# Performance work log

Hardware: AMD Instinct MI355X
Metric: run time of the kernel (lower is better)

## Reference

```python
import jax, jax.numpy as jnp
import numpy as np

DIN = 1024
DOUT = 1024


def setup_inputs() -> dict:
    key = jax.random.key(0)
    kx, kq, kk, kv = jax.random.split(key, 4)
    B, T = 4, 2048
    x = jax.random.normal(kx, (B, T, DIN), dtype=jnp.float32)
    # nn.Linear weights are (dout, din); init like PyTorch default scale
    s = 1.0 / np.sqrt(DIN)
    Wq = jax.random.uniform(kq, (DOUT, DIN), minval=-s, maxval=s, dtype=jnp.float32)
    Wk = jax.random.uniform(kk, (DOUT, DIN), minval=-s, maxval=s, dtype=jnp.float32)
    Wv = jax.random.uniform(kv, (DOUT, DIN), minval=-s, maxval=s, dtype=jnp.float32)
    return {"x": x, "Wq": Wq, "Wk": Wk, "Wv": Wv}


def reference(x, Wq, Wk, Wv):
    B, T, _ = x.shape
    q = jnp.einsum('btd,ed->bte', x, Wq)
    k = jnp.einsum('btd,ed->bte', x, Wk)
    v = jnp.einsum('btd,ed->bte', x, Wv)
    attn = jnp.einsum('bqe,bke->bqk', q, k)  # [B, T, T]
    # Faithful to source: masked_fill result is discarded, so the causal mask
    # is a MULTIPLICATIVE tril of ones (upper triangle logits become 0, not -inf).
    mask = jnp.tril(jnp.ones((T, T), dtype=attn.dtype))
    attn = attn * mask
    # Faithful to source: scale by sqrt(last dim of attn) = sqrt(T), not sqrt(d).
    attn = jax.nn.softmax(attn / jnp.sqrt(jnp.asarray(T, attn.dtype)), axis=-1)
    return jnp.einsum('bqk,bke->bqe', attn, v)
```

## Files before the change

kernel.cpp:

```cpp
#include <hip/hip_runtime.h>
#include <stdint.h>

#define BB 4
#define TT 2048
#define DD 1024
#define NX (BB*TT*DD)
#define NW (DD*DD)
#define SCALE 0.022097086912079608f
#define SCALEI 2.157918643757774e-5f
#define UNSCALE 7.689469810104304e-6f
#define Q8F 2.4606299212598425e-4f

typedef short v8s __attribute__((ext_vector_type(8)));
typedef float v4f __attribute__((ext_vector_type(4)));
typedef int   v4i __attribute__((ext_vector_type(4)));
typedef uint8_t u8;

typedef const void __attribute__((address_space(1))) *as1_cvp;
typedef void __attribute__((address_space(3))) *as3_vp;

__device__ __forceinline__ short f2bf(float f) {
    union { float f; uint32_t u; } x; x.f = f;
    uint32_t r = x.u + 0x7fffu + ((x.u >> 16) & 1u);
    return (short)(r >> 16);
}
__device__ __forceinline__ float bf2f(short s) {
    union { uint32_t u; float f; } x; x.u = ((uint32_t)(uint16_t)s) << 16;
    return x.f;
}

__device__ __forceinline__ void gl_lds16(const void* g, const void* lds_wave_base) {
    __builtin_amdgcn_global_load_lds(
        (as1_cvp)(uintptr_t)g,
        (as3_vp)(uint32_t)(uintptr_t)lds_wave_base,
        16, 0, 0);
}

__device__ __forceinline__ v8s frag_read(const short* lds, int row, int cg) {
    return *(const v8s*)(lds + row * 64 + ((cg ^ (row & 7)) << 3));
}

#define WAITV(N) asm volatile("s_waitcnt vmcnt(" #N ")" ::: "memory")

__device__ __forceinline__ void stage128_512(const short* __restrict__ g, int lda,
                                             short* lds, int tid) {
    #pragma unroll
    for (int s = 0; s < 2; s++) {
        int t = s * 512 + tid;
        int r = t >> 3, c = t & 7, cg = c ^ (r & 7);
        gl_lds16(g + (size_t)r * lda + cg * 8, lds + s * 4096 + (tid >> 6) * 512);
    }
}

__device__ __forceinline__ void stA8(const u8* __restrict__ g, u8* lds, int tid) {
    #pragma unroll
    for (int s = 0; s < 2; s++) {
        int t = s * 512 + tid;
        int r = t >> 3, c = t & 7, cg = c ^ (r & 7);
        gl_lds16(g + (size_t)r * 1024 + cg * 16, lds + s * 8192 + (tid >> 6) * 1024);
    }
}
__device__ __forceinline__ void stB8(const u8* __restrict__ g, u8* lds, int tid, int p) {
    #pragma unroll
    for (int s = 0; s < 2; s++) {
        int t = s * 512 + tid;
        int r = t >> 3, c = t & 7, cg = c ^ (r & 7);
        int grow = ((r >> 5) << 6) + p * 32 + (r & 31);
        gl_lds16(g + (size_t)grow * 1024 + cg * 16, lds + s * 8192 + (tid >> 6) * 1024);
    }
}
__device__ __forceinline__ v4i frag16(const u8* lds, int row, int c) {
    return *(const v4i*)(lds + row * 128 + ((c ^ (row & 7)) << 4));
}

__device__ __forceinline__ void stage64(const u8* __restrict__ g, u8* lds, int tid) {
    int r = tid >> 2, c = tid & 3;
    gl_lds16(g + (size_t)r * 1024 + c * 16, lds + (tid >> 6) * 1024);
}
__device__ __forceinline__ v4i fragK64(const u8* lds, int row, int gq) {
    return *(const v4i*)(lds + row * 64 + gq * 16);
}

__global__ void k_convert(const float* __restrict__ x, const float* __restrict__ Wq,
                          const float* __restrict__ Wk, const float* __restrict__ Wv,
                          u8* __restrict__ dst8, float* __restrict__ rowsum) {
    int i = blockIdx.x * 256 + threadIdx.x;
    if (i < BB * TT) rowsum[i] = (float)((15 - ((i & 2047) >> 7)) * 128);
    size_t base = (size_t)i * 4;
    const float* src; size_t off; float sc; bool clip;
    if (base < NX)               { src = x;  off = base; sc = 32.f; clip = true; }
    else if (base < NX + NW)     { src = Wq; off = base - NX; sc = 4064.f; clip = false; }
    else if (base < NX + 2*(size_t)NW) { src = Wk; off = base - NX - NW; sc = 4064.f; clip = false; }
    else                         { src = Wv; off = base - NX - 2*(size_t)NW; sc = 4064.f; clip = false; }
    float4 f = *(const float4*)(src + off);
    float a0 = f.x * sc, a1 = f.y * sc, a2 = f.z * sc, a3 = f.w * sc;
    if (clip) {
        a0 = fminf(fmaxf(a0, -127.f), 127.f);
        a1 = fminf(fmaxf(a1, -127.f), 127.f);
        a2 = fminf(fmaxf(a2, -127.f), 127.f);
        a3 = fminf(fmaxf(a3, -127.f), 127.f);
    }
    int q0 = __float2int_rn(a0), q1 = __float2int_rn(a1);
    int q2 = __float2int_rn(a2), q3 = __float2int_rn(a3);
    uint32_t w = (uint32_t)(q0 & 255) | ((uint32_t)(q1 & 255) << 8) |
                 ((uint32_t)(q2 & 255) << 16) | ((uint32_t)(q3 & 255) << 24);
    *(uint32_t*)(dst8 + base) = w;
}

__global__ __launch_bounds__(512, 2) void k_qkv(const u8* __restrict__ xb,
                                                const u8* __restrict__ wb,
                                                u8* __restrict__ q8,
                                                u8* __restrict__ k8,
                                                short* __restrict__ vt) {
    int h = blockIdx.x;
    int w = (h & 7) * 96 + (h >> 3);
    int which = w >> 8, rem = w & 255, ntile = rem >> 6, mtile = rem & 63;
    int m0 = mtile * 128, n0 = ntile * 256;
    const u8* Ag = xb + (size_t)m0 * 1024;
    const u8* Bg = wb + (size_t)which * NW + (size_t)n0 * 1024;
    __shared__ __align__(16) u8 SH[98304];
    int tid = threadIdx.x, lane = tid & 63, wave = tid >> 6;
    int wm = wave >> 2, wn = wave & 3;
    int lr = lane & 15, lq = lane >> 4;
    int arow = wm * 64 + lr;
    int brow = wn * 32 + lr;
    v4i acc[4][4];
    #pragma unroll
    for (int i = 0; i < 4; i++)
        #pragma unroll
        for (int j = 0; j < 4; j++) acc[i][j] = (v4i){0, 0, 0, 0};

    stA8(Ag, SH,         tid);
    stB8(Bg, SH + 16384, tid, 0);
    stB8(Bg, SH + 32768, tid, 1);

    #pragma unroll
    for (int t = 0; t < 8; ++t) {
        u8* S  = SH + (t & 1) * 49152;
        u8* Sn = SH + ((t + 1) & 1) * 49152;
        const u8* Agn = Ag + (t + 1) * 128;
        const u8* Bgn = Bg + (t + 1) * 128;
        WAITV(2);
        __builtin_amdgcn_s_barrier();
        v4i af[4][2], bf[2][2];
        #pragma unroll
        for (int i = 0; i < 4; i++)
            #pragma unroll
            for (int kh = 0; kh < 2; kh++) af[i][kh] = frag16(S, arow + i * 16, kh * 4 + lq);
        #pragma unroll
        for (int jj = 0; jj < 2; jj++)
            #pragma unroll
            for (int kh = 0; kh < 2; kh++) bf[jj][kh] = frag16(S + 16384, brow + jj * 16, kh * 4 + lq);
        if (t < 7) {
            stA8(Agn, Sn,         tid);
            stB8(Bgn, Sn + 16384, tid, 0);
        }
        __builtin_amdgcn_s_setprio(1);
        #pragma unroll
        for (int kh = 0; kh < 2; kh++)
            #pragma unroll
            for (int i = 0; i < 4; i++)
                #pragma unroll
                for (int jj = 0; jj < 2; jj++)
                    acc[i][jj] = __builtin_amdgcn_mfma_i32_16x16x64_i8(af[i][kh], bf[jj][kh], acc[i][jj], 0, 0, 0);
        __builtin_amdgcn_s_setprio(0);
        if (t < 7) { WAITV(4); }
        else       { WAITV(0); }
        __builtin_amdgcn_s_barrier();
        v4i bg2[2][2];
        #pragma unroll
        for (int jj = 0; jj < 2; jj++)
            #pragma unroll
            for (int kh = 0; kh < 2; kh++) bg2[jj][kh] = frag16(S + 32768, brow + jj * 16, kh * 4 + lq);
        if (t < 7) stB8(Bgn, Sn + 32768, tid, 1);
        __builtin_amdgcn_s_setprio(1);
        #pragma unroll
        for (int kh = 0; kh < 2; kh++)
            #pragma unroll
            for (int i = 0; i < 4; i++)
                #pragma unroll
                for (int jj = 0; jj < 2; jj++)
                    acc[i][2 + jj] = __builtin_amdgcn_mfma_i32_16x16x64_i8(af[i][kh], bg2[jj][kh], acc[i][2 + jj], 0, 0, 0);
        __builtin_amdgcn_s_setprio(0);
    }

    if (which == 2) {
        #pragma unroll
        for (int a = 0; a < 4; a++)
            #pragma unroll
            for (int b = 0; b < 4; b++)
                #pragma unroll
                for (int r = 0; r < 4; r++) {
                    int row = m0 + wm * 64 + a * 16 + lq * 4 + r;
                    int col = n0 + wn * 64 + b * 16 + lr;
                    int bb = row >> 11, tt2 = row & 2047;
                    vt[((size_t)bb << 21) + ((size_t)col << 11) + tt2] =
                        f2bf((float)acc[a][b][r] * UNSCALE);
                }
    } else {
        u8* outp = (which == 0) ? q8 : k8;
        #pragma unroll
        for (int a = 0; a < 4; a++)
            #pragma unroll
            for (int b = 0; b < 4; b++)
                #pragma unroll
                for (int r = 0; r < 4; r++) {
                    int row = m0 + wm * 64 + a * 16 + lq * 4 + r;
                    int col = n0 + wn * 64 + b * 16 + lr;
                    float v = (float)acc[a][b][r] * Q8F;
                    v = fminf(fmaxf(v, -127.f), 127.f);
                    outp[(size_t)row * 1024 + col] = (u8)(__float2int_rn(v) & 255);
                }
    }
}

__global__ void k_ts1(const short* __restrict__ vt, float* __restrict__ TSpart) {
    int g = blockIdx.x * 256 + threadIdx.x;
    int b = g >> 14, jt = (g >> 10) & 15, e = g & 1023;
    const short* row = vt + ((size_t)b << 21) + ((size_t)e << 11) + jt * 128;
    float s = 0.f;
    #pragma unroll
    for (int c = 0; c < 16; c++) {
        uint4 u = *(const uint4*)(row + c * 8);
        const short* hp = (const short*)&u;
        #pragma unroll
        for (int z = 0; z < 8; z++) s += bf2f(hp[z]);
    }
    TSpart[g] = s;
}
__global__ void k_ts2(const float* __restrict__ TSpart, float* __restrict__ TS) {
    int g = blockIdx.x * 256 + threadIdx.x;
    int b = g >> 10, e = g & 1023;
    float acc = 0.f;
    TS[(size_t)(b * 17 + 16) * 1024 + e] = 0.f;
    for (int jt = 15; jt >= 0; jt--) {
        acc += TSpart[(size_t)(b * 16 + jt) * 1024 + e];
        TS[(size_t)(b * 17 + jt) * 1024 + e] = acc;
    }
}

__global__ __launch_bounds__(512, 4) void k_pk(const u8* __restrict__ q8,
                                               const u8* __restrict__ k8,
                                               short* __restrict__ P,
                                               float* __restrict__ rowsum) {
    int pidx = blockIdx.x, b = blockIdx.z;
    int qt = 0;
    while ((qt + 1) * (qt + 2) / 2 <= pidx) qt++;
    int kt = pidx - qt * (qt + 1) / 2;
    int r0 = qt * 128;
    const u8* Ag = q8 + ((size_t)b * 2048 + r0) * 1024;
    const u8* Bg = k8 + ((size_t)b * 2048 + (size_t)kt * 128) * 1024;
    __shared__ __align__(16) u8 SH[49152];
    int tid = threadIdx.x, lane = tid & 63, wave = tid >> 6;
    int wm2 = wave >> 2, wn4 = wave & 3;
    int lr = lane & 15, lq = lane >> 4;
    v4i acc[4][2];
    #pragma unroll
    for (int i = 0; i < 4; i++)
        #pragma unroll
        for (int j = 0; j < 2; j++) acc[i][j] = (v4i){0, 0, 0, 0};

    stage64(Ag,      SH,                tid);
    stage64(Bg,      SH + 8192,         tid);
    stage64(Ag + 64, SH + 16384,        tid);
    stage64(Bg + 64, SH + 16384 + 8192, tid);

    #pragma unroll
    for (int it = 0; it < 16; ++it) {
        if (it + 1 < 16) { WAITV(2); }
        else             { WAITV(0); }
        __builtin_amdgcn_s_barrier();
        if (it + 2 < 16) {
            u8* Sn = SH + ((it + 2) % 3) * 16384;
            stage64(Ag + (it + 2) * 64, Sn,        tid);
            stage64(Bg + (it + 2) * 64, Sn + 8192, tid);
        }
        const u8* S = SH + (it % 3) * 16384;
        v4i af[4], bf[2];
        #pragma unroll
        for (int i = 0; i < 4; i++) af[i] = fragK64(S, wm2 * 64 + i * 16 + lr, lq);
        #pragma unroll
        for (int j = 0; j < 2; j++) bf[j] = fragK64(S + 8192, wn4 * 32 + j * 16 + lr, lq);
        __builtin_amdgcn_s_setprio(1);
        #pragma unroll
        for (int i = 0; i < 4; i++)
            #pragma unroll
            for (int j = 0; j < 2; j++)
                acc[i][j] = __builtin_amdgcn_mfma_i32_16x16x64_i8(af[i], bf[j], acc[i][j], 0, 0, 0);
        __builtin_amdgcn_s_setprio(0);
    }
    short* Pb = P + ((size_t)b << 22);
    float rs[4][4];
    #pragma unroll
    for (int i = 0; i < 4; i++)
        #pragma unroll
        for (int r = 0; r < 4; r++) rs[i][r] = 0.f;
    #pragma unroll
    for (int i = 0; i < 4; i++)
        #pragma unroll
        for (int j = 0; j < 2; j++)
            #pragma unroll
            for (int r = 0; r < 4; r++) {
                int qi = r0 + wm2 * 64 + i * 16 + lq * 4 + r;
                int kj = kt * 128 + wn4 * 32 + j * 16 + lr;
                float p = (kj <= qi) ? __expf((float)acc[i][j][r] * SCALEI) : 1.0f;
                Pb[(size_t)qi * 2048 + kj] = f2bf(p);
                rs[i][r] += p;
            }
    #pragma unroll
    for (int m = 1; m < 16; m <<= 1)
        #pragma unroll
        for (int i = 0; i < 4; i++)
            #pragma unroll
            for (int r = 0; r < 4; r++) rs[i][r] += __shfl_xor(rs[i][r], m);
    if (lr == 0)
        #pragma unroll
        for (int i = 0; i < 4; i++)
            #pragma unroll
            for (int r = 0; r < 4; r++)
                atomicAdd(&rowsum[b * 2048 + r0 + wm2 * 64 + i * 16 + lq * 4 + r], rs[i][r]);
}

__global__ __launch_bounds__(512, 2) void k_pv(const short* __restrict__ P,
                                               const short* __restrict__ vt,
                                               const float* __restrict__ rowsum,
                                               const float* __restrict__ TS,
                                               float* __restrict__ out) {
    int et = blockIdx.x, p = blockIdx.y, b = blockIdx.z;
    const short* Bg = vt + ((size_t)b << 21) + (size_t)et * 128 * 2048;
    __shared__ __align__(16) short SH[49152];
    int tid = threadIdx.x, lane = tid & 63, wave = tid >> 6;
    int wm2 = wave >> 2, wn4 = wave & 3;
    int lr = lane & 15, lq = lane >> 4;

    #pragma unroll
    for (int ph = 0; ph < 2; ph++) {
        int qt = ph ? p : 15 - p;
        int r0 = qt * 128;
        int iters = 2 * (qt + 1);
        const short* Ag = P + ((size_t)b << 22) + (size_t)r0 * 2048;
        v4f acc[4][2];
        #pragma unroll
        for (int i = 0; i < 4; i++)
            #pragma unroll
            for (int j = 0; j < 2; j++) acc[i][j] = (v4f){0.f, 0.f, 0.f, 0.f};

        stage128_512(Ag,      2048, SH,                tid);
        stage128_512(Bg,      2048, SH + 8192,         tid);
        stage128_512(Ag + 64, 2048, SH + 16384,        tid);
        stage128_512(Bg + 64, 2048, SH + 16384 + 8192, tid);

        for (int it = 0; it < iters; ++it) {
            if (it + 1 < iters) { WAITV(4); }
            else                { WAITV(0); }
            __builtin_amdgcn_s_barrier();
            if (it + 2 < iters) {
                short* Sn = SH + ((it + 2) % 3) * 16384;
                stage128_512(Ag + (it + 2) * 64, 2048, Sn,        tid);
                stage128_512(Bg + (it + 2) * 64, 2048, Sn + 8192, tid);
            }
            short* S = SH + (it % 3) * 16384;
            v8s af[4][2], bf[2][2];
            #pragma unroll
            for (int i = 0; i < 4; i++)
                #pragma unroll
                for (int kk = 0; kk < 2; kk++) af[i][kk] = frag_read(S, wm2 * 64 + i * 16 + lr, kk * 4 + lq);
            #pragma unroll
            for (int j = 0; j < 2; j++)
                #pragma unroll
                for (int kk = 0; kk < 2; kk++) bf[j][kk] = frag_read(S + 8192, wn4 * 32 + j * 16 + lr, kk * 4 + lq);
            __builtin_amdgcn_s_setprio(1);
            #pragma unroll
            for (int kk = 0; kk < 2; kk++)
                #pragma unroll
                for (int i = 0; i < 4; i++)
                    #pragma unroll
                    for (int j = 0; j < 2; j++)
                        acc[i][j] = __builtin_amdgcn_mfma_f32_16x16x32_bf16(af[i][kk], bf[j][kk], acc[i][j], 0, 0, 0);
            __builtin_amdgcn_s_setprio(0);
        }
        const float* tsrow = TS + (size_t)(b * 17 + qt + 1) * 1024;
        #pragma unroll
        for (int i = 0; i < 4; i++)
            #pragma unroll
            for (int j = 0; j < 2; j++)
                #pragma unroll
                for (int r = 0; r < 4; r++) {
                    int row = r0 + wm2 * 64 + i * 16 + lq * 4 + r;
                    int col = et * 128 + wn4 * 32 + j * 16 + lr;
                    float o = (acc[i][j][r] + tsrow[col]) / rowsum[b * 2048 + row];
                    out[((size_t)(b * 2048 + row) << 10) + col] = o;
                }
        __builtin_amdgcn_s_barrier();
    }
}

extern "C" void kernel_launch(void* const* d_in, const int* in_sizes, int n_in,
                              void* d_out, int out_size, void* d_ws, size_t ws_size,
                              hipStream_t stream) {
    const float* x  = (const float*)d_in[0];
    const float* Wq = (const float*)d_in[1];
    const float* Wk = (const float*)d_in[2];
    const float* Wv = (const float*)d_in[3];
    float* out = (float*)d_out;
    char* ws = (char*)d_ws;

    u8*    xb8    = (u8*)(ws + 0);
    u8*    q8     = (u8*)(ws + 11534336);
    u8*    k8     = (u8*)(ws + 19922944);
    short* vt     = (short*)(ws + 28311552);
    short* P      = (short*)(ws + 45088768);
    float* rowsum = (float*)(ws + 78643200);
    float* TSpart = (float*)(ws + 78675968);
    float* TS     = (float*)(ws + 78938112);

    k_convert<<<11264, 256, 0, stream>>>(x, Wq, Wk, Wv, xb8, rowsum);
    k_qkv<<<dim3(768, 1, 1), 512, 0, stream>>>(xb8, xb8 + NX, q8, k8, vt);
    k_ts1<<<256, 256, 0, stream>>>(vt, TSpart);
    k_ts2<<<16, 256, 0, stream>>>(TSpart, TS);
    k_pk<<<dim3(136, 1, 4), 512, 0, stream>>>(q8, k8, P, rowsum);
    k_pv<<<dim3(8, 8, 4), 512, 0, stream>>>(P, vt, rowsum, TS, out);
}
```

Measured before the change: 202.3 us.

## Quantize P and V to int8 and run PV matmul with int8 MFMA

The P matrix written by k_pk is stored as biased int8 (p*64 - 128) instead of bf16. V gets an extra int8 copy scaled by 48, with bias-correction column sums (TQ) computed alongside TS. k_pv then uses i8 MFMA with K=128 per iteration and reconstructs the numerator from the int accumulator, the TQ bias term and TS. This halves the bytes of the P write/read and the PV staging, and uses the faster int8 matrix path. The cost is much coarser quantization of attention weights and values, plus extra stores in the QKV epilogue and k_ts1.

```diff
diff --git a/kernel.cpp b/kernel.cpp
--- a/kernel.cpp
+++ b/kernel.cpp
@@ -10,6 +10,9 @@
 #define SCALEI 2.157918643757774e-5f
 #define UNSCALE 7.689469810104304e-6f
 #define Q8F 2.4606299212598425e-4f
+#define VQ 48.0f
+#define PVF (1.0f/3072.0f)
+#define TQF (1.0f/24.0f)
 
 typedef short v8s __attribute__((ext_vector_type(8)));
 typedef float v4f __attribute__((ext_vector_type(4)));
@@ -27,6 +30,14 @@
 __device__ __forceinline__ float bf2f(short s) {
     union { uint32_t u; float f; } x; x.u = ((uint32_t)(uint16_t)s) << 16;
     return x.f;
+}
+__device__ __forceinline__ int bsum(uint32_t w) {
+#if __has_builtin(__builtin_amdgcn_sdot4)
+    return __builtin_amdgcn_sdot4((int)w, 0x01010101, 0, false);
+#else
+    return (int)(signed char)(w & 255) + (int)(signed char)((w >> 8) & 255) +
+           (int)(signed char)((w >> 16) & 255) + (int)(signed char)((w >> 24) & 255);
+#endif
 }
 
 __device__ __forceinline__ void gl_lds16(const void* g, const void* lds_wave_base) {
@@ -36,28 +47,15 @@
         16, 0, 0);
 }
 
-__device__ __forceinline__ v8s frag_read(const short* lds, int row, int cg) {
-    return *(const v8s*)(lds + row * 64 + ((cg ^ (row & 7)) << 3));
-}
-
 #define WAITV(N) asm volatile("s_waitcnt vmcnt(" #N ")" ::: "memory")
 
-__device__ __forceinline__ void stage128_512(const short* __restrict__ g, int lda,
-                                             short* lds, int tid) {
+__device__ __forceinline__ void stage128B(const u8* __restrict__ g, int lda,
+                                          u8* lds, int tid) {
     #pragma unroll
     for (int s = 0; s < 2; s++) {
         int t = s * 512 + tid;
         int r = t >> 3, c = t & 7, cg = c ^ (r & 7);
-        gl_lds16(g + (size_t)r * lda + cg * 8, lds + s * 4096 + (tid >> 6) * 512);
-    }
-}
-
-__device__ __forceinline__ void stA8(const u8* __restrict__ g, u8* lds, int tid) {
-    #pragma unroll
-    for (int s = 0; s < 2; s++) {
-        int t = s * 512 + tid;
-        int r = t >> 3, c = t & 7, cg = c ^ (r & 7);
-        gl_lds16(g + (size_t)r * 1024 + cg * 16, lds + s * 8192 + (tid >> 6) * 1024);
+        gl_lds16(g + (size_t)r * lda + cg * 16, lds + s * 8192 + (tid >> 6) * 1024);
     }
 }
 __device__ __forceinline__ void stB8(const u8* __restrict__ g, u8* lds, int tid, int p) {
@@ -111,7 +109,8 @@
                                                 const u8* __restrict__ wb,
                                                 u8* __restrict__ q8,
                                                 u8* __restrict__ k8,
-                                                short* __restrict__ vt) {
+                                                short* __restrict__ vt,
+                                                u8* __restrict__ vt8) {
     int h = blockIdx.x;
     int w = (h & 7) * 96 + (h >> 3);
     int which = w >> 8, rem = w & 255, ntile = rem >> 6, mtile = rem & 63;
@@ -130,7 +129,7 @@
         #pragma unroll
         for (int j = 0; j < 4; j++) acc[i][j] = (v4i){0, 0, 0, 0};
 
-    stA8(Ag, SH,         tid);
+    stage128B(Ag, 1024, SH, tid);
     stB8(Bg, SH + 16384, tid, 0);
     stB8(Bg, SH + 32768, tid, 1);
 
@@ -152,7 +151,7 @@
             #pragma unroll
             for (int kh = 0; kh < 2; kh++) bf[jj][kh] = frag16(S + 16384, brow + jj * 16, kh * 4 + lq);
         if (t < 7) {
-            stA8(Agn, Sn,         tid);
+            stage128B(Agn, 1024, Sn,  tid);
             stB8(Bgn, Sn + 16384, tid, 0);
         }
         __builtin_amdgcn_s_setprio(1);
@@ -188,15 +187,25 @@
         #pragma unroll
         for (int a = 0; a < 4; a++)
             #pragma unroll
-            for (int b = 0; b < 4; b++)
-                #pragma unroll
-                for (int r = 0; r < 4; r++) {
-                    int row = m0 + wm * 64 + a * 16 + lq * 4 + r;
-                    int col = n0 + wn * 64 + b * 16 + lr;
-                    int bb = row >> 11, tt2 = row & 2047;
-                    vt[((size_t)bb << 21) + ((size_t)col << 11) + tt2] =
-                        f2bf((float)acc[a][b][r] * UNSCALE);
-                }
+            for (int b = 0; b < 4; b++) {
+                int row0 = m0 + wm * 64 + a * 16 + lq * 4;
+                int col  = n0 + wn * 64 + b * 16 + lr;
+                int bb = row0 >> 11, tt0 = row0 & 2047;
+                size_t idx = ((size_t)bb << 21) + ((size_t)col << 11) + tt0;
+                float v0 = (float)acc[a][b][0] * UNSCALE;
+                float v1 = (float)acc[a][b][1] * UNSCALE;
+                float v2 = (float)acc[a][b][2] * UNSCALE;
+                float v3 = (float)acc[a][b][3] * UNSCALE;
+                short4 hv; hv.x = f2bf(v0); hv.y = f2bf(v1); hv.z = f2bf(v2); hv.w = f2bf(v3);
+                *(short4*)(vt + idx) = hv;
+                int c0 = __float2int_rn(fminf(fmaxf(v0 * VQ, -127.f), 127.f));
+                int c1 = __float2int_rn(fminf(fmaxf(v1 * VQ, -127.f), 127.f));
+                int c2 = __float2int_rn(fminf(fmaxf(v2 * VQ, -127.f), 127.f));
+                int c3 = __float2int_rn(fminf(fmaxf(v3 * VQ, -127.f), 127.f));
+                uint32_t pw = (uint32_t)(c0 & 255) | ((uint32_t)(c1 & 255) << 8) |
+                              ((uint32_t)(c2 & 255) << 16) | ((uint32_t)(c3 & 255) << 24);
+                *(uint32_t*)(vt8 + idx) = pw;
+            }
     } else {
         u8* outp = (which == 0) ? q8 : k8;
         #pragma unroll
@@ -214,7 +223,8 @@
     }
 }
 
-__global__ void k_ts1(const short* __restrict__ vt, float* __restrict__ TSpart) {
+__global__ void k_ts1(const short* __restrict__ vt, const u8* __restrict__ vt8,
+                      float* __restrict__ TSpart, float* __restrict__ TQpart) {
     int g = blockIdx.x * 256 + threadIdx.x;
     int b = g >> 14, jt = (g >> 10) & 15, e = g & 1023;
     const short* row = vt + ((size_t)b << 21) + ((size_t)e << 11) + jt * 128;
@@ -227,8 +237,17 @@
         for (int z = 0; z < 8; z++) s += bf2f(hp[z]);
     }
     TSpart[g] = s;
-}
-__global__ void k_ts2(const float* __restrict__ TSpart, float* __restrict__ TS) {
+    const u8* row8 = vt8 + ((size_t)b << 21) + ((size_t)e << 11) + jt * 128;
+    int si = 0;
+    #pragma unroll
+    for (int c = 0; c < 8; c++) {
+        uint4 u = *(const uint4*)(row8 + c * 16);
+        si += bsum(u.x) + bsum(u.y) + bsum(u.z) + bsum(u.w);
+    }
+    TQpart[g] = (float)si;
+}
+__global__ void k_ts2(const float* __restrict__ TSpart, const float* __restrict__ TQpart,
+                      float* __restrict__ TS, float* __restrict__ TQ) {
     int g = blockIdx.x * 256 + threadIdx.x;
     int b = g >> 10, e = g & 1023;
     float acc = 0.f;
@@ -237,11 +256,17 @@
         acc += TSpart[(size_t)(b * 16 + jt) * 1024 + e];
         TS[(size_t)(b * 17 + jt) * 1024 + e] = acc;
     }
+    float aq = 0.f;
+    TQ[(size_t)(b * 17 + 0) * 1024 + e] = 0.f;
+    for (int jt = 0; jt < 16; jt++) {
+        aq += TQpart[(size_t)(b * 16 + jt) * 1024 + e];
+        TQ[(size_t)(b * 17 + jt + 1) * 1024 + e] = aq;
+    }
 }
 
 __global__ __launch_bounds__(512, 4) void k_pk(const u8* __restrict__ q8,
                                                const u8* __restrict__ k8,
-                                               short* __restrict__ P,
+                                               char* __restrict__ P8,
                                                float* __restrict__ rowsum) {
     int pidx = blockIdx.x, b = blockIdx.z;
     int qt = 0;
@@ -289,7 +314,7 @@
                 acc[i][j] = __builtin_amdgcn_mfma_i32_16x16x64_i8(af[i], bf[j], acc[i][j], 0, 0, 0);
         __builtin_amdgcn_s_setprio(0);
     }
-    short* Pb = P + ((size_t)b << 22);
+    char* Pb = P8 + ((size_t)b << 22);
     float rs[4][4];
     #pragma unroll
     for (int i = 0; i < 4; i++)
@@ -304,8 +329,9 @@
                 int qi = r0 + wm2 * 64 + i * 16 + lq * 4 + r;
                 int kj = kt * 128 + wn4 * 32 + j * 16 + lr;
                 float p = (kj <= qi) ? __expf((float)acc[i][j][r] * SCALEI) : 1.0f;
-                Pb[(size_t)qi * 2048 + kj] = f2bf(p);
-                rs[i][r] += p;
+                int u = __float2int_rn(fminf(p * 64.f, 255.f));
+                Pb[(size_t)qi * 2048 + kj] = (char)(u - 128);
+                rs[i][r] += (float)u * 0.015625f;
             }
     #pragma unroll
     for (int m = 1; m < 16; m <<= 1)
@@ -321,14 +347,15 @@
                 atomicAdd(&rowsum[b * 2048 + r0 + wm2 * 64 + i * 16 + lq * 4 + r], rs[i][r]);
 }
 
-__global__ __launch_bounds__(512, 2) void k_pv(const short* __restrict__ P,
-                                               const short* __restrict__ vt,
+__global__ __launch_bounds__(512, 2) void k_pv(const u8* __restrict__ P8,
+                                               const u8* __restrict__ vt8,
                                                const float* __restrict__ rowsum,
                                                const float* __restrict__ TS,
+                                               const float* __restrict__ TQ,
                                                float* __restrict__ out) {
     int et = blockIdx.x, p = blockIdx.y, b = blockIdx.z;
-    const short* Bg = vt + ((size_t)b << 21) + (size_t)et * 128 * 2048;
-    __shared__ __align__(16) short SH[49152];
+    const u8* Bg = vt8 + ((size_t)b << 21) + (size_t)et * 128 * 2048;
+    __shared__ __align__(16) u8 SH[98304];
     int tid = threadIdx.x, lane = tid & 63, wave = tid >> 6;
     int wm2 = wave >> 2, wn4 = wave & 3;
     int lr = lane & 15, lq = lane >> 4;
@@ -337,49 +364,52 @@
     for (int ph = 0; ph < 2; ph++) {
         int qt = ph ? p : 15 - p;
         int r0 = qt * 128;
-        int iters = 2 * (qt + 1);
-        const short* Ag = P + ((size_t)b << 22) + (size_t)r0 * 2048;
-        v4f acc[4][2];
-        #pragma unroll
-        for (int i = 0; i < 4; i++)
-            #pragma unroll
-            for (int j = 0; j < 2; j++) acc[i][j] = (v4f){0.f, 0.f, 0.f, 0.f};
-
-        stage128_512(Ag,      2048, SH,                tid);
-        stage128_512(Bg,      2048, SH + 8192,         tid);
-        stage128_512(Ag + 64, 2048, SH + 16384,        tid);
-        stage128_512(Bg + 64, 2048, SH + 16384 + 8192, tid);
+        int iters = qt + 1;
+        const u8* Ag = P8 + ((size_t)b << 22) + (size_t)r0 * 2048;
+        v4i acc[4][2];
+        #pragma unroll
+        for (int i = 0; i < 4; i++)
+            #pragma unroll
+            for (int j = 0; j < 2; j++) acc[i][j] = (v4i){0, 0, 0, 0};
+
+        stage128B(Ag, 2048, SH,         tid);
+        stage128B(Bg, 2048, SH + 16384, tid);
+        if (iters > 1) {
+            stage128B(Ag + 128, 2048, SH + 32768,         tid);
+            stage128B(Bg + 128, 2048, SH + 32768 + 16384, tid);
+        }
 
         for (int it = 0; it < iters; ++it) {
             if (it + 1 < iters) { WAITV(4); }
             else                { WAITV(0); }
             __builtin_amdgcn_s_barrier();
             if (it + 2 < iters) {
-                short* Sn = SH + ((it + 2) % 3) * 16384;
-                stage128_512(Ag + (it + 2) * 64, 2048, Sn,        tid);
-                stage128_512(Bg + (it + 2) * 64, 2048, Sn + 8192, tid);
+                u8* Sn = SH + ((it + 2) % 3) * 32768;
+                stage128B(Ag + (it + 2) * 128, 2048, Sn,         tid);
+                stage128B(Bg + (it + 2) * 128, 2048, Sn + 16384, tid);
             }
-            short* S = SH + (it % 3) * 16384;
-            v8s af[4][2], bf[2][2];
+            const u8* S = SH + (it % 3) * 32768;
+            v4i af[4][2], bf[2][2];
             #pragma unroll
             for (int i = 0; i < 4; i++)
                 #pragma unroll
-                for (int kk = 0; kk < 2; kk++) af[i][kk] = frag_read(S, wm2 * 64 + i * 16 + lr, kk * 4 + lq);
+                for (int kh = 0; kh < 2; kh++) af[i][kh] = frag16(S, wm2 * 64 + i * 16 + lr, kh * 4 + lq);
             #pragma unroll
             for (int j = 0; j < 2; j++)
                 #pragma unroll
-                for (int kk = 0; kk < 2; kk++) bf[j][kk] = frag_read(S + 8192, wn4 * 32 + j * 16 + lr, kk * 4 + lq);
+                for (int kh = 0; kh < 2; kh++) bf[j][kh] = frag16(S + 16384, wn4 * 32 + j * 16 + lr, kh * 4 + lq);
             __builtin_amdgcn_s_setprio(1);
             #pragma unroll
-            for (int kk = 0; kk < 2; kk++)
+            for (int kh = 0; kh < 2; kh++)
                 #pragma unroll
                 for (int i = 0; i < 4; i++)
                     #pragma unroll
                     for (int j = 0; j < 2; j++)
-                        acc[i][j] = __builtin_amdgcn_mfma_f32_16x16x32_bf16(af[i][kk], bf[j][kk], acc[i][j], 0, 0, 0);
+                        acc[i][j] = __builtin_amdgcn_mfma_i32_16x16x64_i8(af[i][kh], bf[j][kh], acc[i][j], 0, 0, 0);
             __builtin_amdgcn_s_setprio(0);
         }
         const float* tsrow = TS + (size_t)(b * 17 + qt + 1) * 1024;
+        const float* tqrow = TQ + (size_t)(b * 17 + qt + 1) * 1024;
         #pragma unroll
         for (int i = 0; i < 4; i++)
             #pragma unroll
@@ -388,8 +418,8 @@
                 for (int r = 0; r < 4; r++) {
                     int row = r0 + wm2 * 64 + i * 16 + lq * 4 + r;
                     int col = et * 128 + wn4 * 32 + j * 16 + lr;
-                    float o = (acc[i][j][r] + tsrow[col]) / rowsum[b * 2048 + row];
-                    out[((size_t)(b * 2048 + row) << 10) + col] = o;
+                    float numer = (float)acc[i][j][r] * PVF + tqrow[col] * TQF + tsrow[col];
+                    out[((size_t)(b * 2048 + row) << 10) + col] = numer / rowsum[b * 2048 + row];
                 }
         __builtin_amdgcn_s_barrier();
     }
@@ -409,15 +439,18 @@
     u8*    q8     = (u8*)(ws + 11534336);
     u8*    k8     = (u8*)(ws + 19922944);
     short* vt     = (short*)(ws + 28311552);
-    short* P      = (short*)(ws + 45088768);
-    float* rowsum = (float*)(ws + 78643200);
-    float* TSpart = (float*)(ws + 78675968);
-    float* TS     = (float*)(ws + 78938112);
+    u8*    vt8    = (u8*)(ws + 45088768);
+    char*  P8     = (char*)(ws + 53477376);
+    float* rowsum = (float*)(ws + 70254592);
+    float* TSpart = (float*)(ws + 70287360);
+    float* TS     = (float*)(ws + 70549504);
+    float* TQpart = (float*)(ws + 70828032);
+    float* TQ     = (float*)(ws + 71090176);
 
     k_convert<<<11264, 256, 0, stream>>>(x, Wq, Wk, Wv, xb8, rowsum);
-    k_qkv<<<dim3(768, 1, 1), 512, 0, stream>>>(xb8, xb8 + NX, q8, k8, vt);
-    k_ts1<<<256, 256, 0, stream>>>(vt, TSpart);
-    k_ts2<<<16, 256, 0, stream>>>(TSpart, TS);
-    k_pk<<<dim3(136, 1, 4), 512, 0, stream>>>(q8, k8, P, rowsum);
-    k_pv<<<dim3(8, 8, 4), 512, 0, stream>>>(P, vt, rowsum, TS, out);
-}
+    k_qkv<<<dim3(768, 1, 1), 512, 0, stream>>>(xb8, xb8 + NX, q8, k8, vt, vt8);
+    k_ts1<<<256, 256, 0, stream>>>(vt, vt8, TSpart, TQpart);
+    k_ts2<<<16, 256, 0, stream>>>(TSpart, TQpart, TS, TQ);
+    k_pk<<<dim3(136, 1, 4), 512, 0, stream>>>(q8, k8, P8, rowsum);
+    k_pv<<<dim3(8, 8, 4), 512, 0, stream>>>((const u8*)P8, vt8, rowsum, TS, TQ, out);
+}
```

Result: no change. 204.3 us (+1.0%).
